# Kernel optimization log

Measured on AMD Instinct MI355X. Metric: run time of the kernel, lower is better.

The kernel has to match this reference:

```python
import jax, jax.numpy as jnp
import numpy as np

ATOM_TYPES = (1, 6, 7, 8)  # H, C, N, O
BN_EPS = 1e-3


def setup_inputs() -> dict:
    key = jax.random.key(0)
    k1, k2, k3 = jax.random.split(key, 3)
    B, N, M, d, L = 16, 2048, 64, 3, 12
    X = jax.random.normal(k1, (B, N, d), jnp.float32) * 4.0  # coords in Angstrom-ish scale
    # neighbor indices; offset trick guarantees no self-neighbor (avoids R=0)
    off = jax.random.randint(k2, (B, N, M), 1, N)
    Nbrs = ((jnp.arange(N)[None, :, None] + off) % N).astype(jnp.int32)
    Nbrs_Z = jax.random.randint(k3, (B, N, M), 0, 10).astype(jnp.int32)
    params = np.array([[rc, rs, 4.0] for rc in (4.0, 8.0) for rs in (0.0, 1.0, 2.0, 3.0, 4.0, 5.0)], np.float32)
    rc = jnp.asarray(params[:, 0].reshape(L, 1, 1, 1))
    rs = jnp.asarray(params[:, 1].reshape(L, 1, 1, 1))
    re = jnp.asarray(params[:, 2].reshape(L, 1, 1, 1))
    return {"X": X, "Nbrs": Nbrs, "Nbrs_Z": Nbrs_Z, "rc": rc, "rs": rs, "re": re}


def reference(X, Nbrs, Nbrs_Z, rc, rs, re):
    # gather neighbor coordinates: [B,N,M,d]
    nbr = jax.vmap(lambda coords, idx: coords[idx])(X, Nbrs)
    D = nbr - X[:, :, None, :]                      # displacement tensor [B,N,M,d]
    R = jnp.sqrt(jnp.sum(D * D, axis=-1))           # distance matrix  [B,N,M]
    R1 = R[None]                                    # [1,B,N,M], broadcasts vs [L,1,1,1]
    K = jnp.exp(-re * (R1 - rs) ** 2)               # gaussian        [L,B,N,M]
    FC = jnp.where(R1 <= rc, 0.5 * (jnp.cos(jnp.pi * R1 / rc) + 1.0), 0.0)
    rsf = K * FC                                    # radial symmetry fn [L,B,N,M]
    # per-atom-type masks [A,B,N,M]
    types = jnp.asarray(ATOM_TYPES, Nbrs_Z.dtype)
    conds = (Nbrs_Z[None] == types[:, None, None, None]).astype(rsf.dtype)
    # masked reduce over neighbors, concat over types (type-major) -> [A*L,B,N]
    sym = jnp.einsum('abnm,lbnm->albn', conds, rsf)
    A, L = sym.shape[0], sym.shape[1]
    layer = sym.reshape(A * L, sym.shape[2], sym.shape[3]).transpose(1, 2, 0)  # [B,N,A*L]
    # tf.nn.moments over axis 0 (biased variance) + batch_normalization (no scale/offset)
    m = jnp.mean(layer, axis=0)
    v = jnp.var(layer, axis=0)
    return (layer - m) / jnp.sqrt(v + BN_EPS)
```

## Files before the change

### kernel.cpp

```cpp
#include <hip/hip_runtime.h>

#define NB 16
#define NN 2048
#define NM 64
#define NC 48
#define LDSP 49
#define PIF 3.14159265358979323f

struct F3 { float x, y, z; };

__global__ __launch_bounds__(256) void fused_kernel(
    const float* __restrict__ X,
    const int* __restrict__ Nbrs,
    const int* __restrict__ NbrsZ,
    const float* __restrict__ rcg,
    const float* __restrict__ rsg,
    const float* __restrict__ reg,
    float* __restrict__ out)
{
  __shared__ float sBN[NB * LDSP];

  const int tid = threadIdx.x;
  const int b   = tid >> 4;
  const int t   = tid & 15;
  const int n   = blockIdx.x;
  const int row = b * NN + n;

  const int base = row * NM + t * 4;
  const int4 j4 = *(const int4*)(Nbrs  + base);
  const int4 z4 = *(const int4*)(NbrsZ + base);

  const float rc4 = rcg[0], rc8 = rcg[6];
  const float re  = reg[0];
  const float nre = -re;
  const float pio8  = PIF / rc8;
  const float sp    = rsg[1] - rsg[0];
  const float gcoef = 2.f * re * sp;
  const float rs3   = rsg[3];
  const float qu4 = __expf(nre * (rsg[4] * rsg[4] - rsg[3] * rsg[3]));
  const float qu5 = __expf(nre * (rsg[5] * rsg[5] - rsg[4] * rsg[4]));
  const float qd2 = __expf(nre * (rsg[2] * rsg[2] - rsg[3] * rsg[3]));
  const float qd1 = __expf(nre * (rsg[1] * rsg[1] - rsg[2] * rsg[2]));
  const float qd0 = __expf(nre * (rsg[0] * rsg[0] - rsg[1] * rsg[1]));

  const float* xb = X + (size_t)b * (NN * 3);
  const float xi = xb[n * 3 + 0];
  const float yi = xb[n * 3 + 1];
  const float zi = xb[n * 3 + 2];

  const int js[4] = {j4.x, j4.y, j4.z, j4.w};
  const int zs[4] = {z4.x, z4.y, z4.z, z4.w};

  float px[4], py[4], pz[4];
#pragma unroll
  for (int u = 0; u < 4; ++u) {
    const F3 p = *(const F3*)(xb + js[u] * 3);
    px[u] = p.x;
    py[u] = p.y;
    pz[u] = p.z;
  }

  float2 acc2[24];
#pragma unroll
  for (int c = 0; c < 24; ++c) acc2[c] = make_float2(0.f, 0.f);

#pragma unroll
  for (int u = 0; u < 4; ++u) {
    const float dx = px[u] - xi, dy = py[u] - yi, dz = pz[u] - zi;
    const float R = sqrtf(fmaf(dx, dx, fmaf(dy, dy, dz * dz)));
    const float Rk = fminf(R, rc8);

    const float u3 = Rk - rs3;
    const float K3 = __expf(nre * (u3 * u3));
    const float Gu = __expf(gcoef * Rk);
    const float Gd = __builtin_amdgcn_rcpf(Gu);
    const float K4 = K3 * Gu * qu4;
    const float K5 = K4 * Gu * qu5;
    const float K2 = K3 * Gd * qd2;
    const float K1 = K2 * Gd * qd1;
    const float K0 = K1 * Gd * qd0;
    const float K[6] = {K0, K1, K2, K3, K4, K5};

    const float c8  = __cosf(pio8 * R);
    const float c4  = fmaf(c8 + c8, c8, -1.f);
    const float fc8 = (R <= rc8) ? fmaf(0.5f, c8, 0.5f) : 0.f;
    const float fc4 = (R <= rc4) ? fmaf(0.5f, c4, 0.5f) : 0.f;

    const int z = zs[u];
    const float a40 = (z == 1) ? fc4 : 0.f, a80 = (z == 1) ? fc8 : 0.f;
    const float a41 = (z == 6) ? fc4 : 0.f, a81 = (z == 6) ? fc8 : 0.f;
    const float a42 = (z == 7) ? fc4 : 0.f, a82 = (z == 7) ? fc8 : 0.f;
    const float a43 = (z == 8) ? fc4 : 0.f, a83 = (z == 8) ? fc8 : 0.f;

#pragma unroll
    for (int r = 0; r < 6; ++r) {
      const float k = K[r];
      acc2[ 0 + r].x = fmaf(a40, k, acc2[ 0 + r].x);
      acc2[ 0 + r].y = fmaf(a80, k, acc2[ 0 + r].y);
      acc2[ 6 + r].x = fmaf(a41, k, acc2[ 6 + r].x);
      acc2[ 6 + r].y = fmaf(a81, k, acc2[ 6 + r].y);
      acc2[12 + r].x = fmaf(a42, k, acc2[12 + r].x);
      acc2[12 + r].y = fmaf(a82, k, acc2[12 + r].y);
      acc2[18 + r].x = fmaf(a43, k, acc2[18 + r].x);
      acc2[18 + r].y = fmaf(a83, k, acc2[18 + r].y);
    }
  }

  float acc[NC];
#pragma unroll
  for (int ty = 0; ty < 4; ++ty)
#pragma unroll
    for (int r = 0; r < 6; ++r) {
      acc[ty * 12 + r]     = acc2[ty * 6 + r].x;
      acc[ty * 12 + 6 + r] = acc2[ty * 6 + r].y;
    }

#pragma unroll
  for (int c = 0; c < NC; ++c) acc[c] += __shfl_xor(acc[c], 8, 64);
  const bool s8 = (t & 8) != 0;
#pragma unroll
  for (int j = 0; j < 24; ++j) acc[j] = s8 ? acc[24 + j] : acc[j];
#pragma unroll
  for (int j = 0; j < 24; ++j) acc[j] += __shfl_xor(acc[j], 4, 64);
  const bool s4 = (t & 4) != 0;
#pragma unroll
  for (int j = 0; j < 12; ++j) acc[j] = s4 ? acc[12 + j] : acc[j];
#pragma unroll
  for (int j = 0; j < 12; ++j) acc[j] += __shfl_xor(acc[j], 2, 64);
  const bool s2 = (t & 2) != 0;
#pragma unroll
  for (int j = 0; j < 6; ++j) acc[j] = s2 ? acc[6 + j] : acc[j];
#pragma unroll
  for (int j = 0; j < 6; ++j) acc[j] += __shfl_xor(acc[j], 1, 64);
  const bool s1 = (t & 1) != 0;
#pragma unroll
  for (int j = 0; j < 3; ++j) acc[j] = s1 ? acc[3 + j] : acc[j];

  const int lb = b * LDSP + 3 * t;
  sBN[lb + 0] = acc[0];
  sBN[lb + 1] = acc[1];
  sBN[lb + 2] = acc[2];

  __syncthreads();

  if (tid < NC) {
    const int cc = tid;
    float x[NB];
    float s = 0.f;
#pragma unroll
    for (int bb = 0; bb < NB; ++bb) {
      x[bb] = sBN[bb * LDSP + cc];
      s += x[bb];
    }
    const float mean = s * (1.f / NB);
    float vs = 0.f;
#pragma unroll
    for (int bb = 0; bb < NB; ++bb) {
      const float d = x[bb] - mean;
      vs = fmaf(d, d, vs);
    }
    const float inv = rsqrtf(vs * (1.f / NB) + 1e-3f);
#pragma unroll
    for (int bb = 0; bb < NB; ++bb) {
      out[(size_t)bb * (NN * NC) + n * NC + cc] = (x[bb] - mean) * inv;
    }
  }
}

extern "C" void kernel_launch(void* const* d_in, const int* in_sizes, int n_in,
                              void* d_out, int out_size, void* d_ws, size_t ws_size,
                              hipStream_t stream) {
  const float* X   = (const float*)d_in[0];
  const int* Nbrs  = (const int*)d_in[1];
  const int* NbrsZ = (const int*)d_in[2];
  const float* rcg = (const float*)d_in[3];
  const float* rsg = (const float*)d_in[4];
  const float* reg = (const float*)d_in[5];

  float* out = (float*)d_out;

  fused_kernel<<<2048, 256, 0, stream>>>(X, Nbrs, NbrsZ, rcg, rsg, reg, out);
}
```

Measured before the change: 18.37 us.

## Split accumulation into two cutoff passes to cut register pressure

The 48-channel accumulation is split into two passes, one per cutoff radius, each holding 24 accumulators and running its own shuffle reduction before writing its part of the LDS tile. Launch bounds now request 8 blocks per SM to push the compiler toward fewer VGPRs and higher occupancy. The Gaussian terms and cosine are recomputed in each pass, and the rc4 cutoff now uses its own cosine instead of the double-angle identity, adding transcendental work and shuffle rounds.

After: 22.22 us. 20.9% more time.

```diff
diff --git a/kernel.cpp b/kernel.cpp
--- a/kernel.cpp
+++ b/kernel.cpp
@@ -9,7 +9,93 @@
 
 struct F3 { float x, y, z; };
 
-__global__ __launch_bounds__(256) void fused_kernel(
+__device__ __forceinline__ void rc_pass(
+    const float R[4], const int zs[4],
+    float rcX, float pioX, float rc8, int grp,
+    float nre, float gcoef, float rs3,
+    float qu4, float qu5, float qd2, float qd1, float qd0,
+    int b, int t, float* __restrict__ sBN)
+{
+  float2 acc2[12];
+#pragma unroll
+  for (int q = 0; q < 12; ++q) acc2[q] = make_float2(0.f, 0.f);
+
+#pragma unroll
+  for (int u = 0; u < 4; ++u) {
+    const float Rv = R[u];
+    const float Rk = fminf(Rv, rc8);
+
+    const float u3 = Rk - rs3;
+    const float K3 = __expf(nre * (u3 * u3));
+    const float Gu = __expf(gcoef * Rk);
+    const float Gd = __builtin_amdgcn_rcpf(Gu);
+    const float K4 = K3 * Gu * qu4;
+    const float K5 = K4 * Gu * qu5;
+    const float K2 = K3 * Gd * qd2;
+    const float K1 = K2 * Gd * qd1;
+    const float K0 = K1 * Gd * qd0;
+    const float K[6] = {K0, K1, K2, K3, K4, K5};
+
+    const float cX  = __cosf(pioX * Rv);
+    const float fcX = (Rv <= rcX) ? fmaf(0.5f, cX, 0.5f) : 0.f;
+
+    const int z = zs[u];
+    const float a0 = (z == 1) ? fcX : 0.f;
+    const float a1 = (z == 6) ? fcX : 0.f;
+    const float a2 = (z == 7) ? fcX : 0.f;
+    const float a3 = (z == 8) ? fcX : 0.f;
+
+#pragma unroll
+    for (int p = 0; p < 3; ++p) {
+      const float k0 = K[2 * p], k1 = K[2 * p + 1];
+      acc2[0 + p].x = fmaf(a0, k0, acc2[0 + p].x);
+      acc2[0 + p].y = fmaf(a0, k1, acc2[0 + p].y);
+      acc2[3 + p].x = fmaf(a1, k0, acc2[3 + p].x);
+      acc2[3 + p].y = fmaf(a1, k1, acc2[3 + p].y);
+      acc2[6 + p].x = fmaf(a2, k0, acc2[6 + p].x);
+      acc2[6 + p].y = fmaf(a2, k1, acc2[6 + p].y);
+      acc2[9 + p].x = fmaf(a3, k0, acc2[9 + p].x);
+      acc2[9 + p].y = fmaf(a3, k1, acc2[9 + p].y);
+    }
+  }
+
+  float acc[24];
+#pragma unroll
+  for (int q = 0; q < 12; ++q) {
+    acc[2 * q]     = acc2[q].x;
+    acc[2 * q + 1] = acc2[q].y;
+  }
+
+#pragma unroll
+  for (int c = 0; c < 24; ++c) acc[c] += __shfl_xor(acc[c], 8, 64);
+  const bool s8 = (t & 8) != 0;
+#pragma unroll
+  for (int j = 0; j < 12; ++j) acc[j] = s8 ? acc[12 + j] : acc[j];
+#pragma unroll
+  for (int j = 0; j < 12; ++j) acc[j] += __shfl_xor(acc[j], 4, 64);
+  const bool s4 = (t & 4) != 0;
+#pragma unroll
+  for (int j = 0; j < 6; ++j) acc[j] = s4 ? acc[6 + j] : acc[j];
+#pragma unroll
+  for (int j = 0; j < 6; ++j) acc[j] += __shfl_xor(acc[j], 2, 64);
+  const bool s2 = (t & 2) != 0;
+#pragma unroll
+  for (int j = 0; j < 3; ++j) acc[j] = s2 ? acc[3 + j] : acc[j];
+#pragma unroll
+  for (int j = 0; j < 3; ++j) acc[j] += __shfl_xor(acc[j], 1, 64);
+
+  const int ty = 2 * ((t >> 3) & 1) + ((t >> 2) & 1);
+  const int r0 = 3 * ((t >> 1) & 1);
+  const int gb = b * LDSP + ty * 12 + grp * 6 + r0;
+  if (t & 1) {
+    sBN[gb + 2] = acc[2];
+  } else {
+    sBN[gb + 0] = acc[0];
+    sBN[gb + 1] = acc[1];
+  }
+}
+
+__global__ __launch_bounds__(256, 8) void fused_kernel(
     const float* __restrict__ X,
     const int* __restrict__ Nbrs,
     const int* __restrict__ NbrsZ,
@@ -33,6 +119,7 @@
   const float rc4 = rcg[0], rc8 = rcg[6];
   const float re  = reg[0];
   const float nre = -re;
+  const float pio4  = PIF / rc4;
   const float pio8  = PIF / rc8;
   const float sp    = rsg[1] - rsg[0];
   const float gcoef = 2.f * re * sp;
@@ -51,95 +138,18 @@
   const int js[4] = {j4.x, j4.y, j4.z, j4.w};
   const int zs[4] = {z4.x, z4.y, z4.z, z4.w};
 
-  float px[4], py[4], pz[4];
+  float R[4];
 #pragma unroll
   for (int u = 0; u < 4; ++u) {
     const F3 p = *(const F3*)(xb + js[u] * 3);
-    px[u] = p.x;
-    py[u] = p.y;
-    pz[u] = p.z;
+    const float dx = p.x - xi, dy = p.y - yi, dz = p.z - zi;
+    R[u] = sqrtf(fmaf(dx, dx, fmaf(dy, dy, dz * dz)));
   }
 
-  float2 acc2[24];
-#pragma unroll
-  for (int c = 0; c < 24; ++c) acc2[c] = make_float2(0.f, 0.f);
-
-#pragma unroll
-  for (int u = 0; u < 4; ++u) {
-    const float dx = px[u] - xi, dy = py[u] - yi, dz = pz[u] - zi;
-    const float R = sqrtf(fmaf(dx, dx, fmaf(dy, dy, dz * dz)));
-    const float Rk = fminf(R, rc8);
-
-    const float u3 = Rk - rs3;
-    const float K3 = __expf(nre * (u3 * u3));
-    const float Gu = __expf(gcoef * Rk);
-    const float Gd = __builtin_amdgcn_rcpf(Gu);
-    const float K4 = K3 * Gu * qu4;
-    const float K5 = K4 * Gu * qu5;
-    const float K2 = K3 * Gd * qd2;
-    const float K1 = K2 * Gd * qd1;
-    const float K0 = K1 * Gd * qd0;
-    const float K[6] = {K0, K1, K2, K3, K4, K5};
-
-    const float c8  = __cosf(pio8 * R);
-    const float c4  = fmaf(c8 + c8, c8, -1.f);
-    const float fc8 = (R <= rc8) ? fmaf(0.5f, c8, 0.5f) : 0.f;
-    const float fc4 = (R <= rc4) ? fmaf(0.5f, c4, 0.5f) : 0.f;
-
-    const int z = zs[u];
-    const float a40 = (z == 1) ? fc4 : 0.f, a80 = (z == 1) ? fc8 : 0.f;
-    const float a41 = (z == 6) ? fc4 : 0.f, a81 = (z == 6) ? fc8 : 0.f;
-    const float a42 = (z == 7) ? fc4 : 0.f, a82 = (z == 7) ? fc8 : 0.f;
-    const float a43 = (z == 8) ? fc4 : 0.f, a83 = (z == 8) ? fc8 : 0.f;
-
-#pragma unroll
-    for (int r = 0; r < 6; ++r) {
-      const float k = K[r];
-      acc2[ 0 + r].x = fmaf(a40, k, acc2[ 0 + r].x);
-      acc2[ 0 + r].y = fmaf(a80, k, acc2[ 0 + r].y);
-      acc2[ 6 + r].x = fmaf(a41, k, acc2[ 6 + r].x);
-      acc2[ 6 + r].y = fmaf(a81, k, acc2[ 6 + r].y);
-      acc2[12 + r].x = fmaf(a42, k, acc2[12 + r].x);
-      acc2[12 + r].y = fmaf(a82, k, acc2[12 + r].y);
-      acc2[18 + r].x = fmaf(a43, k, acc2[18 + r].x);
-      acc2[18 + r].y = fmaf(a83, k, acc2[18 + r].y);
-    }
-  }
-
-  float acc[NC];
-#pragma unroll
-  for (int ty = 0; ty < 4; ++ty)
-#pragma unroll
-    for (int r = 0; r < 6; ++r) {
-      acc[ty * 12 + r]     = acc2[ty * 6 + r].x;
-      acc[ty * 12 + 6 + r] = acc2[ty * 6 + r].y;
-    }
-
-#pragma unroll
-  for (int c = 0; c < NC; ++c) acc[c] += __shfl_xor(acc[c], 8, 64);
-  const bool s8 = (t & 8) != 0;
-#pragma unroll
-  for (int j = 0; j < 24; ++j) acc[j] = s8 ? acc[24 + j] : acc[j];
-#pragma unroll
-  for (int j = 0; j < 24; ++j) acc[j] += __shfl_xor(acc[j], 4, 64);
-  const bool s4 = (t & 4) != 0;
-#pragma unroll
-  for (int j = 0; j < 12; ++j) acc[j] = s4 ? acc[12 + j] : acc[j];
-#pragma unroll
-  for (int j = 0; j < 12; ++j) acc[j] += __shfl_xor(acc[j], 2, 64);
-  const bool s2 = (t & 2) != 0;
-#pragma unroll
-  for (int j = 0; j < 6; ++j) acc[j] = s2 ? acc[6 + j] : acc[j];
-#pragma unroll
-  for (int j = 0; j < 6; ++j) acc[j] += __shfl_xor(acc[j], 1, 64);
-  const bool s1 = (t & 1) != 0;
-#pragma unroll
-  for (int j = 0; j < 3; ++j) acc[j] = s1 ? acc[3 + j] : acc[j];
-
-  const int lb = b * LDSP + 3 * t;
-  sBN[lb + 0] = acc[0];
-  sBN[lb + 1] = acc[1];
-  sBN[lb + 2] = acc[2];
+  rc_pass(R, zs, rc4, pio4, rc8, 0, nre, gcoef, rs3,
+          qu4, qu5, qd2, qd1, qd0, b, t, sBN);
+  rc_pass(R, zs, rc8, pio8, rc8, 1, nre, gcoef, rs3,
+          qu4, qu5, qd2, qd1, qd0, b, t, sBN);
 
   __syncthreads();
 
```
